# Kernel optimization log

Measured on AMD Instinct MI355X. Metric: run time of the kernel, lower is better.

## Reference

```python
import jax, jax.numpy as jnp
import numpy as np

N_HEAD = 16
N_KV_HEAD = 4
HEAD_DIM = 128
RMS_EPS = 1.1920928955078125e-07  # torch float32 eps used by F.rms_norm default


def apply_rotary_emb(x, cos, sin):
    # x: [B,T,H,D]; cos/sin: [1,T,1,D/2]
    d = x.shape[-1] // 2
    x1, x2 = x[..., :d], x[..., d:]
    return jnp.concatenate([x1 * cos + x2 * sin, -x1 * sin + x2 * cos], axis=-1)


def rms_norm(x):
    return x * jax.lax.rsqrt(jnp.mean(x * x, axis=-1, keepdims=True) + RMS_EPS)


def setup_inputs() -> dict:
    key = jax.random.key(0)
    ks = jax.random.split(key, 7)
    B, T, C = 2, 2048, 2048
    return {
        "x": jax.random.normal(ks[0], (B, T, C), jnp.float32),
        "cos": jax.random.normal(ks[1], (1, T, 1, HEAD_DIM // 2), jnp.float32),
        "sin": jax.random.normal(ks[2], (1, T, 1, HEAD_DIM // 2), jnp.float32),
        "wq": jax.random.normal(ks[3], (C, N_HEAD * HEAD_DIM), jnp.float32) * 0.02,
        "wk": jax.random.normal(ks[4], (C, N_KV_HEAD * HEAD_DIM), jnp.float32) * 0.02,
        "wv": jax.random.normal(ks[5], (C, N_KV_HEAD * HEAD_DIM), jnp.float32) * 0.02,
        "wo": jax.random.normal(ks[6], (C, C), jnp.float32) * 0.02,
        "window_size": 512,
    }


def reference(x, cos, sin, wq, wk, wv, wo, window_size):
    B, T, C = x.shape
    H, KV, D = N_HEAD, N_KV_HEAD, HEAD_DIM
    rep = H // KV
    q = (x @ wq).reshape(B, T, H, D)
    k = (x @ wk).reshape(B, T, KV, D)
    v = (x @ wv).reshape(B, T, KV, D)
    q = rms_norm(apply_rotary_emb(q, cos, sin))
    k = rms_norm(apply_rotary_emb(k, cos, sin))
    # GQA: group query heads by kv head instead of materializing expanded K/V
    qg = q.reshape(B, T, KV, rep, D)
    scale = 1.0 / np.sqrt(D)
    scores = jnp.einsum('btkrd,bskd->bkrts', qg, k) * scale  # [B,KV,rep,T,S]
    row = jnp.arange(T)[:, None]
    col = jnp.arange(T)[None, :]
    mask = (col <= row) & (row - col <= window_size)  # causal & sliding window
    scores = jnp.where(mask, scores, jnp.finfo(scores.dtype).min)
    probs = jax.nn.softmax(scores, axis=-1)
    y = jnp.einsum('bkrts,bskd->btkrd', probs, v).reshape(B, T, H * D)
    return y @ wo
```

## Files before the change

kernel.cpp:

```cpp
#include <hip/hip_runtime.h>
#include <stdint.h>

typedef __attribute__((ext_vector_type(4))) float f32x4;
typedef __attribute__((ext_vector_type(8))) __bf16 bf16x8;
typedef __attribute__((ext_vector_type(4))) unsigned int u32x4;
typedef unsigned short u16;

#define B_DIM 2
#define T_DIM 2048
#define C_DIM 2048
#define H_Q   16
#define H_KV  4
#define HD    128
#define NQKV  3072
#define MTOK  4096
#define RMS_EPS 1.1920928955078125e-07f

__device__ __forceinline__ u16 f2bf(float f) {
  union { float f; unsigned int u; } v; v.f = f;
  unsigned int r = v.u + 0x7FFFu + ((v.u >> 16) & 1u);
  return (u16)(r >> 16);
}
__device__ __forceinline__ float bf2f(u16 h) {
  union { unsigned int u; float f; } v; v.u = ((unsigned int)h) << 16;
  return v.f;
}
__device__ __forceinline__ f32x4 mfma16(bf16x8 a, bf16x8 b, f32x4 c) {
  return __builtin_amdgcn_mfma_f32_16x16x32_bf16(a, b, c, 0, 0, 0);
}
__device__ __forceinline__ void gl_lds16(const void* g, void* l) {
  __builtin_amdgcn_global_load_lds(
      (const __attribute__((address_space(1))) unsigned int*)g,
      (__attribute__((address_space(3))) unsigned int*)l, 16, 0, 0);
}

__global__ __launch_bounds__(256) void cast_x_kernel(const float* __restrict__ x,
                                                     u16* __restrict__ xb, int n) {
  int i = (blockIdx.x * 256 + threadIdx.x) * 4;
  if (i >= n) return;
  float4 v = *(const float4*)(x + i);
  u16 o0 = f2bf(v.x), o1 = f2bf(v.y), o2 = f2bf(v.z), o3 = f2bf(v.w);
  unsigned int lo = (unsigned int)o0 | ((unsigned int)o1 << 16);
  unsigned int hi = (unsigned int)o2 | ((unsigned int)o3 << 16);
  *(uint2*)(xb + i) = make_uint2(lo, hi);
}

__global__ __launch_bounds__(256) void transpose_all_kernel(const float* __restrict__ wq,
                                                            const float* __restrict__ wk,
                                                            const float* __restrict__ wv,
                                                            const float* __restrict__ wo,
                                                            u16* __restrict__ wqkvb,
                                                            u16* __restrict__ wob) {
  __shared__ float tile[64][65];
  int nb = blockIdx.x, kb = blockIdx.y;
  const float* src; u16* dst; int srcN, nloc;
  if (nb < 32)      { src = wq; srcN = 2048; nloc = nb;      dst = wqkvb; }
  else if (nb < 40) { src = wk; srcN = 512;  nloc = nb - 32; dst = wqkvb + (size_t)2048 * 2048; }
  else if (nb < 48) { src = wv; srcN = 512;  nloc = nb - 40; dst = wqkvb + (size_t)2560 * 2048; }
  else              { src = wo; srcN = 2048; nloc = nb - 48; dst = wob; }
  int n0 = nloc * 64, k0 = kb * 64;
  int t = threadIdx.x;
  #pragma unroll
  for (int idx = t; idx < 4096; idx += 256) {
    int r = idx >> 6, c = idx & 63;
    tile[r][c] = src[(size_t)(k0 + r) * srcN + n0 + c];
  }
  __syncthreads();
  #pragma unroll
  for (int idx = t; idx < 4096; idx += 256) {
    int r = idx >> 6, c = idx & 63;
    dst[(size_t)(n0 + r) * 2048 + k0 + c] = f2bf(tile[c][r]);
  }
}

__global__ __launch_bounds__(256) void rope_rms_kernel(u16* __restrict__ qkv,
                                                       const float* __restrict__ cosb,
                                                       const float* __restrict__ sinb) {
  int gw = (blockIdx.x * 256 + threadIdx.x) >> 6;
  int lane = threadIdx.x & 63;
  int hh = gw % (H_Q + H_KV);
  int tok = gw / (H_Q + H_KV);
  int t = tok & (T_DIM - 1);
  int base = (hh < H_Q) ? hh * HD : (C_DIM + (hh - H_Q) * HD);
  u16* p = qkv + (size_t)tok * NQKV + base;
  float x1 = bf2f(p[lane]);
  float x2 = bf2f(p[lane + 64]);
  float c = cosb[t * 64 + lane];
  float s = sinb[t * 64 + lane];
  float o1 =  x1 * c + x2 * s;
  float o2 = -x1 * s + x2 * c;
  float ss = o1 * o1 + o2 * o2;
  #pragma unroll
  for (int off = 1; off < 64; off <<= 1) ss += __shfl_xor(ss, off);
  float r = rsqrtf(ss * (1.0f / 128.0f) + RMS_EPS);
  p[lane]      = f2bf(o1 * r);
  p[lane + 64] = f2bf(o2 * r);
}

__global__ __launch_bounds__(256) void vtrans_kernel(const u16* __restrict__ qkv,
                                                     u16* __restrict__ vt) {
  __shared__ __align__(16) u16 tile[64][136];
  int bid = blockIdx.x;
  int tt0 = (bid & 31) * 64;
  int kvh = (bid >> 5) & 3;
  int b   = bid >> 7;
  const u16* vp = qkv + ((size_t)b * T_DIM + tt0) * NQKV + C_DIM + H_KV * HD + kvh * HD;
  int tid = threadIdx.x;
  #pragma unroll
  for (int i = 0; i < 4; ++i) {
    int cid = tid + i * 256;
    int r = cid >> 4, c = cid & 15;
    u32x4 v = *(const u32x4*)(vp + (size_t)r * NQKV + c * 8);
    *(u32x4*)&tile[r][c * 8] = v;
  }
  __syncthreads();
  u16* op = vt + ((size_t)(b * H_KV + kvh) * HD) * T_DIM + tt0;
  #pragma unroll
  for (int i = 0; i < 4; ++i) {
    int cid = tid + i * 256;
    int d = cid >> 3, tc = cid & 7;
    u16 vals[8];
    #pragma unroll
    for (int j = 0; j < 8; ++j) vals[j] = tile[tc * 8 + j][d];
    u32x4 w;
    w.x = (unsigned int)vals[0] | ((unsigned int)vals[1] << 16);
    w.y = (unsigned int)vals[2] | ((unsigned int)vals[3] << 16);
    w.z = (unsigned int)vals[4] | ((unsigned int)vals[5] << 16);
    w.w = (unsigned int)vals[6] | ((unsigned int)vals[7] << 16);
    *(u32x4*)(op + (size_t)d * T_DIM + tc * 8) = w;
  }
}

template<int BF16OUT>
__global__ __launch_bounds__(256) void gemm_bt_kernel(const u16* __restrict__ A,
                                                      const u16* __restrict__ Bt,
                                                      void* __restrict__ Cv,
                                                      int M, int N, int K) {
  __shared__ __align__(16) u16 Asm[128 * 64];
  __shared__ __align__(16) u16 Bsm[128 * 64];
  const int tid = threadIdx.x;
  const int lane = tid & 63;
  const int wid = tid >> 6;
  const int m0 = blockIdx.y * 128, n0 = blockIdx.x * 128;
  const int wm = (wid >> 1) * 64, wn = (wid & 1) * 64;
  const int l15 = lane & 15, l4 = lane >> 4;
  const int csrc = (lane & 7) ^ (lane >> 3);
  f32x4 acc[4][4] = {};

  for (int k0 = 0; k0 < K; k0 += 64) {
    __syncthreads();
    #pragma unroll
    for (int i = 0; i < 4; ++i) {
      int g = wid * 4 + i;
      int row = g * 8 + (lane >> 3);
      gl_lds16(A  + (size_t)(m0 + row) * K + k0 + csrc * 8, (char*)Asm + g * 1024);
      gl_lds16(Bt + (size_t)(n0 + row) * K + k0 + csrc * 8, (char*)Bsm + g * 1024);
    }
    __syncthreads();
    #pragma unroll
    for (int ks = 0; ks < 2; ++ks) {
      bf16x8 af[4], bfr[4];
      #pragma unroll
      for (int mf = 0; mf < 4; ++mf) {
        int r = wm + mf * 16 + l15;
        int bo = r * 128 + (((ks * 4 + l4) ^ (r & 7)) * 16);
        af[mf] = __builtin_bit_cast(bf16x8, *(const u32x4*)((const char*)Asm + bo));
      }
      #pragma unroll
      for (int nf = 0; nf < 4; ++nf) {
        int r = wn + nf * 16 + l15;
        int bo = r * 128 + (((ks * 4 + l4) ^ (r & 7)) * 16);
        bfr[nf] = __builtin_bit_cast(bf16x8, *(const u32x4*)((const char*)Bsm + bo));
      }
      #pragma unroll
      for (int mf = 0; mf < 4; ++mf)
        #pragma unroll
        for (int nf = 0; nf < 4; ++nf)
          acc[mf][nf] = mfma16(af[mf], bfr[nf], acc[mf][nf]);
    }
  }
  #pragma unroll
  for (int mf = 0; mf < 4; ++mf)
    #pragma unroll
    for (int nf = 0; nf < 4; ++nf)
      #pragma unroll
      for (int reg = 0; reg < 4; ++reg) {
        int row = m0 + wm + mf * 16 + l4 * 4 + reg;
        int col = n0 + wn + nf * 16 + l15;
        float v = acc[mf][nf][reg];
        if (BF16OUT) ((u16*)Cv)[(size_t)row * N + col] = f2bf(v);
        else         ((float*)Cv)[(size_t)row * N + col] = v;
      }
}

__global__ __launch_bounds__(256) void attn_kernel(const u16* __restrict__ qkv,
                                                   const u16* __restrict__ vt,
                                                   u16* __restrict__ yb,
                                                   const int* __restrict__ wsz_p) {
  __shared__ __align__(16) u16 Ksm[64 * 128];
  __shared__ __align__(16) u16 Vsm[128 * 64];
  __shared__ __align__(16) u16 Psm[4 * 16 * 64];

  const int W = wsz_p[0];
  const int tid = threadIdx.x, lane = tid & 63, wid = tid >> 6;
  const int l15 = lane & 15, l4 = lane >> 4;
  const int bid = blockIdx.x;
  const int h   = bid & 15;
  const int b   = (bid >> 4) & 1;
  const int qt  = 31 - (bid >> 5);
  const int kvh = h >> 2;
  const size_t tokb = (size_t)b * T_DIM;
  const u16* vtb = vt + ((size_t)(b * H_KV + kvh) * HD) * T_DIM;
  const int rbase = qt * 64 + wid * 16;

  bf16x8 qf[4];
  {
    int r = rbase + l15;
    const u16* qp = qkv + (tokb + r) * NQKV + h * HD;
    #pragma unroll
    for (int ks = 0; ks < 4; ++ks)
      qf[ks] = __builtin_bit_cast(bf16x8, *(const u32x4*)(qp + ks * 32 + l4 * 8));
  }

  f32x4 yacc[8] = {};
  float mrow[4], lrow[4];
  #pragma unroll
  for (int rg = 0; rg < 4; ++rg) { mrow[rg] = -3.0e38f; lrow[rg] = 0.0f; }

  const float sc = 0.08838834764831845f * 1.4426950408889634f;
  int smin = qt * 64 - W; if (smin < 0) smin = 0;
  const int t0 = smin >> 6;
  char* pbase = (char*)Psm + wid * 2048;

  for (int kt = t0; kt <= qt; ++kt) {
    __syncthreads();
    {
      const u16* kp = qkv + (tokb + kt * 64) * NQKV + C_DIM + kvh * HD;
      #pragma unroll
      for (int i = 0; i < 4; ++i) {
        int g = wid * 4 + i;
        int row = g * 4 + (lane >> 4);
        int cs = (lane & 15) ^ (row & 15);
        gl_lds16(kp + (size_t)row * NQKV + cs * 8, (char*)Ksm + g * 1024);
      }
    }
    {
      const u16* vp = vtb + kt * 64;
      #pragma unroll
      for (int i = 0; i < 4; ++i) {
        int g = wid * 4 + i;
        int d = g * 8 + (lane >> 3);
        int cs = (lane & 7) ^ (d & 7);
        gl_lds16(vp + (size_t)d * T_DIM + cs * 8, (char*)Vsm + g * 1024);
      }
    }
    __syncthreads();

    const int slo = kt * 64;
    bool active = (slo <= rbase + 15) && ((rbase - (slo + 63)) <= W);
    if (active) {
      float Sc[4][4];
      #pragma unroll
      for (int nf = 0; nf < 4; ++nf) {
        f32x4 sa = {0.f, 0.f, 0.f, 0.f};
        int key = nf * 16 + l15;
        #pragma unroll
        for (int ks = 0; ks < 4; ++ks) {
          int bo = key * 256 + (((ks * 4 + l4) ^ (key & 15)) * 16);
          bf16x8 kf = __builtin_bit_cast(bf16x8, *(const u32x4*)((const char*)Ksm + bo));
          sa = mfma16(qf[ks], kf, sa);
        }
        #pragma unroll
        for (int rg = 0; rg < 4; ++rg) Sc[nf][rg] = sa[rg] * sc;
      }
      bool fullvalid = ((slo + 63) <= rbase) && ((rbase + 15 - slo) <= W);
      if (!fullvalid) {
        #pragma unroll
        for (int nf = 0; nf < 4; ++nf) {
          int s = slo + nf * 16 + l15;
          #pragma unroll
          for (int rg = 0; rg < 4; ++rg) {
            int r = rbase + l4 * 4 + rg;
            if (s > r || (r - s) > W) Sc[nf][rg] = -3.0e38f;
          }
        }
      }
      float fmul[4];
      #pragma unroll
      for (int rg = 0; rg < 4; ++rg) {
        float tm = fmaxf(fmaxf(Sc[0][rg], Sc[1][rg]), fmaxf(Sc[2][rg], Sc[3][rg]));
        #pragma unroll
        for (int off = 1; off < 16; off <<= 1) tm = fmaxf(tm, __shfl_xor(tm, off));
        float mnew = fmaxf(mrow[rg], tm);
        float mo = fmaxf(mrow[rg], -1.0e30f);
        float mc = fmaxf(mnew,     -1.0e30f);
        fmul[rg] = exp2f(mo - mc);
        mrow[rg] = mnew;
      }
      float rs[4] = {0.f, 0.f, 0.f, 0.f};
      #pragma unroll
      for (int nf = 0; nf < 4; ++nf)
        #pragma unroll
        for (int rg = 0; rg < 4; ++rg) {
          float mc = fmaxf(mrow[rg], -1.0e30f);
          float pv = exp2f(Sc[nf][rg] - mc);
          rs[rg] += pv;
          int q   = l4 * 4 + rg;
          int key = nf * 16 + l15;
          int bo = q * 128 + (((key >> 3) ^ (q & 7)) * 16) + (key & 7) * 2;
          *(u16*)(pbase + bo) = f2bf(pv);
        }
      #pragma unroll
      for (int rg = 0; rg < 4; ++rg) {
        #pragma unroll
        for (int off = 1; off < 16; off <<= 1) rs[rg] += __shfl_xor(rs[rg], off);
        lrow[rg] = lrow[rg] * fmul[rg] + rs[rg];
      }
      f32x4 fv = {fmul[0], fmul[1], fmul[2], fmul[3]};
      #pragma unroll
      for (int nf2 = 0; nf2 < 8; ++nf2) yacc[nf2] *= fv;

      #pragma unroll
      for (int ks2 = 0; ks2 < 2; ++ks2) {
        int qr = l15;
        int boA = qr * 128 + (((ks2 * 4 + l4) ^ (qr & 7)) * 16);
        bf16x8 pa = __builtin_bit_cast(bf16x8, *(const u32x4*)(pbase + boA));
        #pragma unroll
        for (int nf2 = 0; nf2 < 8; ++nf2) {
          int d = nf2 * 16 + l15;
          int boB = d * 128 + (((ks2 * 4 + l4) ^ (d & 7)) * 16);
          bf16x8 vf = __builtin_bit_cast(bf16x8, *(const u32x4*)((const char*)Vsm + boB));
          yacc[nf2] = mfma16(pa, vf, yacc[nf2]);
        }
      }
    }
  }

  #pragma unroll
  for (int nf2 = 0; nf2 < 8; ++nf2)
    #pragma unroll
    for (int rg = 0; rg < 4; ++rg) {
      int r = rbase + l4 * 4 + rg;
      float v = yacc[nf2][rg] / lrow[rg];
      yb[(tokb + r) * (size_t)C_DIM + h * HD + nf2 * 16 + l15] = f2bf(v);
    }
}

extern "C" void kernel_launch(void* const* d_in, const int* in_sizes, int n_in,
                              void* d_out, int out_size, void* d_ws, size_t ws_size,
                              hipStream_t stream) {
  const float* x    = (const float*)d_in[0];
  const float* cosb = (const float*)d_in[1];
  const float* sinb = (const float*)d_in[2];
  const float* wq   = (const float*)d_in[3];
  const float* wk   = (const float*)d_in[4];
  const float* wv   = (const float*)d_in[5];
  const float* wo   = (const float*)d_in[6];
  const int*   wsz  = (const int*)d_in[7];

  char* ws = (char*)d_ws;
  u16* xb    = (u16*)(ws);
  u16* qkvb  = (u16*)(ws + (size_t)16777216);
  u16* wqkvb = (u16*)(ws + (size_t)41943040);
  u16* wob   = (u16*)(ws + (size_t)54525952);
  u16* ybuf  = (u16*)(ws + (size_t)62914560);
  u16* vtb   = (u16*)(ws);

  cast_x_kernel<<<8192, 256, 0, stream>>>(x, xb, MTOK * C_DIM);
  transpose_all_kernel<<<dim3(80, 32), 256, 0, stream>>>(wq, wk, wv, wo, wqkvb, wob);

  gemm_bt_kernel<1><<<dim3(NQKV / 128, MTOK / 128), 256, 0, stream>>>(xb, wqkvb, qkvb, MTOK, NQKV, C_DIM);
  rope_rms_kernel<<<(MTOK * (H_Q + H_KV)) / 4, 256, 0, stream>>>(qkvb, cosb, sinb);
  vtrans_kernel<<<B_DIM * H_KV * (T_DIM / 64), 256, 0, stream>>>(qkvb, vtb);
  attn_kernel<<<B_DIM * H_Q * (T_DIM / 64), 256, 0, stream>>>(qkvb, vtb, ybuf, wsz);
  gemm_bt_kernel<0><<<dim3(C_DIM / 128, MTOK / 128), 256, 0, stream>>>(ybuf, wob, d_out, MTOK, C_DIM, C_DIM);
}
```

Measured before the change: 198.6 us.

## Merge prep/rope kernels and make attention read K/V directly from global

Fuses the x cast with the weight transpose, and the RoPE+RMS pass with the V transpose, into two combined launches. This cuts kernel launches from seven to five. The attention kernel drops its shared-memory K/V staging and block-wide barriers. Each wave now loads K and V fragments straight from global memory over its own key-tile range, with setprio hints around the MFMA sections. This removes the syncs and the shared-memory traffic, but relies on L2/L1 for K/V reuse across the four waves, which may raise global memory traffic.

```diff
diff --git a/kernel.cpp b/kernel.cpp
--- a/kernel.cpp
+++ b/kernel.cpp
@@ -34,100 +34,100 @@
       (__attribute__((address_space(3))) unsigned int*)l, 16, 0, 0);
 }
 
-__global__ __launch_bounds__(256) void cast_x_kernel(const float* __restrict__ x,
-                                                     u16* __restrict__ xb, int n) {
-  int i = (blockIdx.x * 256 + threadIdx.x) * 4;
-  if (i >= n) return;
-  float4 v = *(const float4*)(x + i);
-  u16 o0 = f2bf(v.x), o1 = f2bf(v.y), o2 = f2bf(v.z), o3 = f2bf(v.w);
-  unsigned int lo = (unsigned int)o0 | ((unsigned int)o1 << 16);
-  unsigned int hi = (unsigned int)o2 | ((unsigned int)o3 << 16);
-  *(uint2*)(xb + i) = make_uint2(lo, hi);
-}
-
-__global__ __launch_bounds__(256) void transpose_all_kernel(const float* __restrict__ wq,
-                                                            const float* __restrict__ wk,
-                                                            const float* __restrict__ wv,
-                                                            const float* __restrict__ wo,
-                                                            u16* __restrict__ wqkvb,
-                                                            u16* __restrict__ wob) {
+__global__ __launch_bounds__(256) void prep_kernel(const float* __restrict__ x,
+                                                   const float* __restrict__ wq,
+                                                   const float* __restrict__ wk,
+                                                   const float* __restrict__ wv,
+                                                   const float* __restrict__ wo,
+                                                   u16* __restrict__ xb,
+                                                   u16* __restrict__ wqkvb,
+                                                   u16* __restrict__ wob) {
   __shared__ float tile[64][65];
-  int nb = blockIdx.x, kb = blockIdx.y;
-  const float* src; u16* dst; int srcN, nloc;
-  if (nb < 32)      { src = wq; srcN = 2048; nloc = nb;      dst = wqkvb; }
-  else if (nb < 40) { src = wk; srcN = 512;  nloc = nb - 32; dst = wqkvb + (size_t)2048 * 2048; }
-  else if (nb < 48) { src = wv; srcN = 512;  nloc = nb - 40; dst = wqkvb + (size_t)2560 * 2048; }
-  else              { src = wo; srcN = 2048; nloc = nb - 48; dst = wob; }
-  int n0 = nloc * 64, k0 = kb * 64;
-  int t = threadIdx.x;
-  #pragma unroll
-  for (int idx = t; idx < 4096; idx += 256) {
-    int r = idx >> 6, c = idx & 63;
-    tile[r][c] = src[(size_t)(k0 + r) * srcN + n0 + c];
-  }
-  __syncthreads();
-  #pragma unroll
-  for (int idx = t; idx < 4096; idx += 256) {
-    int r = idx >> 6, c = idx & 63;
-    dst[(size_t)(n0 + r) * 2048 + k0 + c] = f2bf(tile[c][r]);
-  }
-}
-
-__global__ __launch_bounds__(256) void rope_rms_kernel(u16* __restrict__ qkv,
-                                                       const float* __restrict__ cosb,
-                                                       const float* __restrict__ sinb) {
-  int gw = (blockIdx.x * 256 + threadIdx.x) >> 6;
-  int lane = threadIdx.x & 63;
-  int hh = gw % (H_Q + H_KV);
-  int tok = gw / (H_Q + H_KV);
-  int t = tok & (T_DIM - 1);
-  int base = (hh < H_Q) ? hh * HD : (C_DIM + (hh - H_Q) * HD);
-  u16* p = qkv + (size_t)tok * NQKV + base;
-  float x1 = bf2f(p[lane]);
-  float x2 = bf2f(p[lane + 64]);
-  float c = cosb[t * 64 + lane];
-  float s = sinb[t * 64 + lane];
-  float o1 =  x1 * c + x2 * s;
-  float o2 = -x1 * s + x2 * c;
-  float ss = o1 * o1 + o2 * o2;
-  #pragma unroll
-  for (int off = 1; off < 64; off <<= 1) ss += __shfl_xor(ss, off);
-  float r = rsqrtf(ss * (1.0f / 128.0f) + RMS_EPS);
-  p[lane]      = f2bf(o1 * r);
-  p[lane + 64] = f2bf(o2 * r);
-}
-
-__global__ __launch_bounds__(256) void vtrans_kernel(const u16* __restrict__ qkv,
+  int bid = blockIdx.x, t = threadIdx.x;
+  if (bid < 2560) {
+    int nb = bid % 80, kb = bid / 80;
+    const float* src; u16* dst; int srcN, nloc;
+    if (nb < 32)      { src = wq; srcN = 2048; nloc = nb;      dst = wqkvb; }
+    else if (nb < 40) { src = wk; srcN = 512;  nloc = nb - 32; dst = wqkvb + (size_t)2048 * 2048; }
+    else if (nb < 48) { src = wv; srcN = 512;  nloc = nb - 40; dst = wqkvb + (size_t)2560 * 2048; }
+    else              { src = wo; srcN = 2048; nloc = nb - 48; dst = wob; }
+    int n0 = nloc * 64, k0 = kb * 64;
+    #pragma unroll
+    for (int idx = t; idx < 4096; idx += 256) {
+      int r = idx >> 6, c = idx & 63;
+      tile[r][c] = src[(size_t)(k0 + r) * srcN + n0 + c];
+    }
+    __syncthreads();
+    #pragma unroll
+    for (int idx = t; idx < 4096; idx += 256) {
+      int r = idx >> 6, c = idx & 63;
+      dst[(size_t)(n0 + r) * 2048 + k0 + c] = f2bf(tile[c][r]);
+    }
+  } else {
+    int i = ((bid - 2560) * 256 + t) * 4;
+    if (i >= MTOK * C_DIM) return;
+    float4 v = *(const float4*)(x + i);
+    u16 o0 = f2bf(v.x), o1 = f2bf(v.y), o2 = f2bf(v.z), o3 = f2bf(v.w);
+    unsigned int lo = (unsigned int)o0 | ((unsigned int)o1 << 16);
+    unsigned int hi = (unsigned int)o2 | ((unsigned int)o3 << 16);
+    *(uint2*)(xb + i) = make_uint2(lo, hi);
+  }
+}
+
+__global__ __launch_bounds__(256) void ropevt_kernel(u16* __restrict__ qkv,
+                                                     const float* __restrict__ cosb,
+                                                     const float* __restrict__ sinb,
                                                      u16* __restrict__ vt) {
   __shared__ __align__(16) u16 tile[64][136];
-  int bid = blockIdx.x;
-  int tt0 = (bid & 31) * 64;
-  int kvh = (bid >> 5) & 3;
-  int b   = bid >> 7;
-  const u16* vp = qkv + ((size_t)b * T_DIM + tt0) * NQKV + C_DIM + H_KV * HD + kvh * HD;
-  int tid = threadIdx.x;
-  #pragma unroll
-  for (int i = 0; i < 4; ++i) {
-    int cid = tid + i * 256;
-    int r = cid >> 4, c = cid & 15;
-    u32x4 v = *(const u32x4*)(vp + (size_t)r * NQKV + c * 8);
-    *(u32x4*)&tile[r][c * 8] = v;
-  }
-  __syncthreads();
-  u16* op = vt + ((size_t)(b * H_KV + kvh) * HD) * T_DIM + tt0;
-  #pragma unroll
-  for (int i = 0; i < 4; ++i) {
-    int cid = tid + i * 256;
-    int d = cid >> 3, tc = cid & 7;
-    u16 vals[8];
-    #pragma unroll
-    for (int j = 0; j < 8; ++j) vals[j] = tile[tc * 8 + j][d];
-    u32x4 w;
-    w.x = (unsigned int)vals[0] | ((unsigned int)vals[1] << 16);
-    w.y = (unsigned int)vals[2] | ((unsigned int)vals[3] << 16);
-    w.z = (unsigned int)vals[4] | ((unsigned int)vals[5] << 16);
-    w.w = (unsigned int)vals[6] | ((unsigned int)vals[7] << 16);
-    *(u32x4*)(op + (size_t)d * T_DIM + tc * 8) = w;
+  int bid = blockIdx.x, tid = threadIdx.x;
+  if (bid < 256) {
+    int tt0 = (bid & 31) * 64;
+    int kvh = (bid >> 5) & 3;
+    int b   = bid >> 7;
+    const u16* vp = qkv + ((size_t)b * T_DIM + tt0) * NQKV + C_DIM + H_KV * HD + kvh * HD;
+    #pragma unroll
+    for (int i = 0; i < 4; ++i) {
+      int cid = tid + i * 256;
+      int r = cid >> 4, c = cid & 15;
+      u32x4 v = *(const u32x4*)(vp + (size_t)r * NQKV + c * 8);
+      *(u32x4*)&tile[r][c * 8] = v;
+    }
+    __syncthreads();
+    u16* op = vt + ((size_t)(b * H_KV + kvh) * HD) * T_DIM + tt0;
+    #pragma unroll
+    for (int i = 0; i < 4; ++i) {
+      int cid = tid + i * 256;
+      int d = cid >> 3, tc = cid & 7;
+      u16 vals[8];
+      #pragma unroll
+      for (int j = 0; j < 8; ++j) vals[j] = tile[tc * 8 + j][d];
+      u32x4 w;
+      w.x = (unsigned int)vals[0] | ((unsigned int)vals[1] << 16);
+      w.y = (unsigned int)vals[2] | ((unsigned int)vals[3] << 16);
+      w.z = (unsigned int)vals[4] | ((unsigned int)vals[5] << 16);
+      w.w = (unsigned int)vals[6] | ((unsigned int)vals[7] << 16);
+      *(u32x4*)(op + (size_t)d * T_DIM + tc * 8) = w;
+    }
+  } else {
+    int gw = ((bid - 256) * 256 + tid) >> 6;
+    int lane = tid & 63;
+    int hh = gw % (H_Q + H_KV);
+    int tok = gw / (H_Q + H_KV);
+    int t = tok & (T_DIM - 1);
+    int base = (hh < H_Q) ? hh * HD : (C_DIM + (hh - H_Q) * HD);
+    u16* p = qkv + (size_t)tok * NQKV + base;
+    float x1 = bf2f(p[lane]);
+    float x2 = bf2f(p[lane + 64]);
+    float c = cosb[t * 64 + lane];
+    float s = sinb[t * 64 + lane];
+    float o1 =  x1 * c + x2 * s;
+    float o2 = -x1 * s + x2 * c;
+    float ss = o1 * o1 + o2 * o2;
+    #pragma unroll
+    for (int off = 1; off < 64; off <<= 1) ss += __shfl_xor(ss, off);
+    float r = rsqrtf(ss * (1.0f / 128.0f) + RMS_EPS);
+    p[lane]      = f2bf(o1 * r);
+    p[lane + 64] = f2bf(o2 * r);
   }
 }
 
@@ -197,8 +197,6 @@
                                                    const u16* __restrict__ vt,
                                                    u16* __restrict__ yb,
                                                    const int* __restrict__ wsz_p) {
-  __shared__ __align__(16) u16 Ksm[64 * 128];
-  __shared__ __align__(16) u16 Vsm[128 * 64];
   __shared__ __align__(16) u16 Psm[4 * 16 * 64];
 
   const int W = wsz_p[0];
@@ -211,6 +209,7 @@
   const int kvh = h >> 2;
   const size_t tokb = (size_t)b * T_DIM;
   const u16* vtb = vt + ((size_t)(b * H_KV + kvh) * HD) * T_DIM;
+  const u16* kb  = qkv + tokb * NQKV + C_DIM + kvh * HD;
   const int rbase = qt * 64 + wid * 16;
 
   bf16x8 qf[4];
@@ -228,111 +227,89 @@
   for (int rg = 0; rg < 4; ++rg) { mrow[rg] = -3.0e38f; lrow[rg] = 0.0f; }
 
   const float sc = 0.08838834764831845f * 1.4426950408889634f;
-  int smin = qt * 64 - W; if (smin < 0) smin = 0;
+  int smin = rbase - W; if (smin < 0) smin = 0;
   const int t0 = smin >> 6;
+  const int t1 = (rbase + 15) >> 6;
   char* pbase = (char*)Psm + wid * 2048;
 
-  for (int kt = t0; kt <= qt; ++kt) {
-    __syncthreads();
-    {
-      const u16* kp = qkv + (tokb + kt * 64) * NQKV + C_DIM + kvh * HD;
-      #pragma unroll
-      for (int i = 0; i < 4; ++i) {
-        int g = wid * 4 + i;
-        int row = g * 4 + (lane >> 4);
-        int cs = (lane & 15) ^ (row & 15);
-        gl_lds16(kp + (size_t)row * NQKV + cs * 8, (char*)Ksm + g * 1024);
-      }
-    }
-    {
-      const u16* vp = vtb + kt * 64;
-      #pragma unroll
-      for (int i = 0; i < 4; ++i) {
-        int g = wid * 4 + i;
-        int d = g * 8 + (lane >> 3);
-        int cs = (lane & 7) ^ (d & 7);
-        gl_lds16(vp + (size_t)d * T_DIM + cs * 8, (char*)Vsm + g * 1024);
-      }
-    }
-    __syncthreads();
-
+  for (int kt = t0; kt <= t1; ++kt) {
     const int slo = kt * 64;
-    bool active = (slo <= rbase + 15) && ((rbase - (slo + 63)) <= W);
-    if (active) {
-      float Sc[4][4];
+    float Sc[4][4];
+    __builtin_amdgcn_s_setprio(1);
+    #pragma unroll
+    for (int nf = 0; nf < 4; ++nf) {
+      f32x4 sa = {0.f, 0.f, 0.f, 0.f};
+      const u16* krow = kb + (size_t)(slo + nf * 16 + l15) * NQKV;
+      #pragma unroll
+      for (int ks = 0; ks < 4; ++ks) {
+        bf16x8 kf = __builtin_bit_cast(bf16x8, *(const u32x4*)(krow + ks * 32 + l4 * 8));
+        sa = mfma16(qf[ks], kf, sa);
+      }
+      #pragma unroll
+      for (int rg = 0; rg < 4; ++rg) Sc[nf][rg] = sa[rg] * sc;
+    }
+    __builtin_amdgcn_s_setprio(0);
+
+    bool fullvalid = ((slo + 63) <= rbase) && ((rbase + 15 - slo) <= W);
+    if (!fullvalid) {
       #pragma unroll
       for (int nf = 0; nf < 4; ++nf) {
-        f32x4 sa = {0.f, 0.f, 0.f, 0.f};
-        int key = nf * 16 + l15;
-        #pragma unroll
-        for (int ks = 0; ks < 4; ++ks) {
-          int bo = key * 256 + (((ks * 4 + l4) ^ (key & 15)) * 16);
-          bf16x8 kf = __builtin_bit_cast(bf16x8, *(const u32x4*)((const char*)Ksm + bo));
-          sa = mfma16(qf[ks], kf, sa);
-        }
-        #pragma unroll
-        for (int rg = 0; rg < 4; ++rg) Sc[nf][rg] = sa[rg] * sc;
-      }
-      bool fullvalid = ((slo + 63) <= rbase) && ((rbase + 15 - slo) <= W);
-      if (!fullvalid) {
-        #pragma unroll
-        for (int nf = 0; nf < 4; ++nf) {
-          int s = slo + nf * 16 + l15;
-          #pragma unroll
-          for (int rg = 0; rg < 4; ++rg) {
-            int r = rbase + l4 * 4 + rg;
-            if (s > r || (r - s) > W) Sc[nf][rg] = -3.0e38f;
-          }
-        }
-      }
-      float fmul[4];
-      #pragma unroll
-      for (int rg = 0; rg < 4; ++rg) {
-        float tm = fmaxf(fmaxf(Sc[0][rg], Sc[1][rg]), fmaxf(Sc[2][rg], Sc[3][rg]));
-        #pragma unroll
-        for (int off = 1; off < 16; off <<= 1) tm = fmaxf(tm, __shfl_xor(tm, off));
-        float mnew = fmaxf(mrow[rg], tm);
-        float mo = fmaxf(mrow[rg], -1.0e30f);
-        float mc = fmaxf(mnew,     -1.0e30f);
-        fmul[rg] = exp2f(mo - mc);
-        mrow[rg] = mnew;
-      }
-      float rs[4] = {0.f, 0.f, 0.f, 0.f};
-      #pragma unroll
-      for (int nf = 0; nf < 4; ++nf)
+        int s = slo + nf * 16 + l15;
         #pragma unroll
         for (int rg = 0; rg < 4; ++rg) {
-          float mc = fmaxf(mrow[rg], -1.0e30f);
-          float pv = exp2f(Sc[nf][rg] - mc);
-          rs[rg] += pv;
-          int q   = l4 * 4 + rg;
-          int key = nf * 16 + l15;
-          int bo = q * 128 + (((key >> 3) ^ (q & 7)) * 16) + (key & 7) * 2;
-          *(u16*)(pbase + bo) = f2bf(pv);
+          int r = rbase + l4 * 4 + rg;
+          if (s > r || (r - s) > W) Sc[nf][rg] = -3.0e38f;
         }
+      }
+    }
+    float fmul[4];
+    #pragma unroll
+    for (int rg = 0; rg < 4; ++rg) {
+      float tm = fmaxf(fmaxf(Sc[0][rg], Sc[1][rg]), fmaxf(Sc[2][rg], Sc[3][rg]));
+      #pragma unroll
+      for (int off = 1; off < 16; off <<= 1) tm = fmaxf(tm, __shfl_xor(tm, off));
+      float mnew = fmaxf(mrow[rg], tm);
+      float mo = fmaxf(mrow[rg], -1.0e30f);
+      float mc = fmaxf(mnew,     -1.0e30f);
+      fmul[rg] = exp2f(mo - mc);
+      mrow[rg] = mnew;
+    }
+    float rs[4] = {0.f, 0.f, 0.f, 0.f};
+    #pragma unroll
+    for (int nf = 0; nf < 4; ++nf)
       #pragma unroll
       for (int rg = 0; rg < 4; ++rg) {
-        #pragma unroll
-        for (int off = 1; off < 16; off <<= 1) rs[rg] += __shfl_xor(rs[rg], off);
-        lrow[rg] = lrow[rg] * fmul[rg] + rs[rg];
-      }
-      f32x4 fv = {fmul[0], fmul[1], fmul[2], fmul[3]};
-      #pragma unroll
-      for (int nf2 = 0; nf2 < 8; ++nf2) yacc[nf2] *= fv;
-
-      #pragma unroll
-      for (int ks2 = 0; ks2 < 2; ++ks2) {
-        int qr = l15;
-        int boA = qr * 128 + (((ks2 * 4 + l4) ^ (qr & 7)) * 16);
-        bf16x8 pa = __builtin_bit_cast(bf16x8, *(const u32x4*)(pbase + boA));
-        #pragma unroll
-        for (int nf2 = 0; nf2 < 8; ++nf2) {
-          int d = nf2 * 16 + l15;
-          int boB = d * 128 + (((ks2 * 4 + l4) ^ (d & 7)) * 16);
-          bf16x8 vf = __builtin_bit_cast(bf16x8, *(const u32x4*)((const char*)Vsm + boB));
-          yacc[nf2] = mfma16(pa, vf, yacc[nf2]);
-        }
-      }
+        float mc = fmaxf(mrow[rg], -1.0e30f);
+        float pv = exp2f(Sc[nf][rg] - mc);
+        rs[rg] += pv;
+        int q   = l4 * 4 + rg;
+        int key = nf * 16 + l15;
+        int bo = q * 128 + (((key >> 3) ^ (q & 7)) * 16) + (key & 7) * 2;
+        *(u16*)(pbase + bo) = f2bf(pv);
+      }
+    #pragma unroll
+    for (int rg = 0; rg < 4; ++rg) {
+      #pragma unroll
+      for (int off = 1; off < 16; off <<= 1) rs[rg] += __shfl_xor(rs[rg], off);
+      lrow[rg] = lrow[rg] * fmul[rg] + rs[rg];
+    }
+    f32x4 fv = {fmul[0], fmul[1], fmul[2], fmul[3]};
+    #pragma unroll
+    for (int nf2 = 0; nf2 < 8; ++nf2) yacc[nf2] *= fv;
+
+    const u16* vrow = vtb + slo;
+    #pragma unroll
+    for (int ks2 = 0; ks2 < 2; ++ks2) {
+      int boA = l15 * 128 + (((ks2 * 4 + l4) ^ (l15 & 7)) * 16);
+      bf16x8 pa = __builtin_bit_cast(bf16x8, *(const u32x4*)(pbase + boA));
+      __builtin_amdgcn_s_setprio(1);
+      #pragma unroll
+      for (int nf2 = 0; nf2 < 8; ++nf2) {
+        bf16x8 vf = __builtin_bit_cast(bf16x8,
+            *(const u32x4*)(vrow + (size_t)(nf2 * 16 + l15) * T_DIM + ks2 * 32 + l4 * 8));
+        yacc[nf2] = mfma16(pa, vf, yacc[nf2]);
+      }
+      __builtin_amdgcn_s_setprio(0);
     }
   }
 
@@ -366,12 +343,9 @@
   u16* ybuf  = (u16*)(ws + (size_t)62914560);
   u16* vtb   = (u16*)(ws);
 
-  cast_x_kernel<<<8192, 256, 0, stream>>>(x, xb, MTOK * C_DIM);
-  transpose_all_kernel<<<dim3(80, 32), 256, 0, stream>>>(wq, wk, wv, wo, wqkvb, wob);
-
+  prep_kernel<<<2560 + 8192, 256, 0, stream>>>(x, wq, wk, wv, wo, xb, wqkvb, wob);
   gemm_bt_kernel<1><<<dim3(NQKV / 128, MTOK / 128), 256, 0, stream>>>(xb, wqkvb, qkvb, MTOK, NQKV, C_DIM);
-  rope_rms_kernel<<<(MTOK * (H_Q + H_KV)) / 4, 256, 0, stream>>>(qkvb, cosb, sinb);
-  vtrans_kernel<<<B_DIM * H_KV * (T_DIM / 64), 256, 0, stream>>>(qkvb, vtb);
+  ropevt_kernel<<<256 + (MTOK * (H_Q + H_KV)) / 4, 256, 0, stream>>>(qkvb, cosb, sinb, vtb);
   attn_kernel<<<B_DIM * H_Q * (T_DIM / 64), 256, 0, stream>>>(qkvb, vtb, ybuf, wsz);
   gemm_bt_kernel<0><<<dim3(C_DIM / 128, MTOK / 128), 256, 0, stream>>>(ybuf, wob, d_out, MTOK, C_DIM, C_DIM);
 }
```

Measured after the change: 269.3 us. 1.36x slower.
